# Kernel optimization log

Hardware: AMD Instinct MI355X
Metric: run time of the kernel (lower is better)

Reference implementation:

```python
import jax, jax.numpy as jnp
import numpy as np


def setup_inputs() -> dict:
    key = jax.random.key(0)
    ks = jax.random.split(key, 5)
    B, T, D, U = 32, 2048, 512, 512
    scale = 1.0 / np.sqrt(D)
    return {
        "full": jax.random.normal(ks[0], (B, T, D), jnp.float32),
        "last": jax.random.normal(ks[1], (B, D), jnp.float32),
        "W1": jax.random.normal(ks[2], (D, U), jnp.float32) * scale,
        "b1": jnp.zeros((U,), jnp.float32),
        "W2": jax.random.normal(ks[3], (D, U), jnp.float32) * scale,
        "b2": jnp.zeros((U,), jnp.float32),
        "V": jax.random.normal(ks[4], (U, 1), jnp.float32) * (1.0 / np.sqrt(U)),
        "bV": jnp.zeros((1,), jnp.float32),
    }


def reference(full, last, W1, b1, W2, b2, V, bV):
    # full: [B,T,D], last: [B,D]
    h1 = jnp.einsum("btd,du->btu", full, W1) + b1          # [B,T,U]
    h2 = last @ W2 + b2                                      # [B,U]
    score = jnp.tanh(h1 + h2[:, None, :]) @ V + bV           # [B,T,1]
    attn = jax.nn.softmax(score, axis=1)                     # [B,T,1]
    context = jnp.sum(attn * full, axis=1)                   # [B,D]
    return context
```

## Files before the change

### kernel.cpp

```cpp
#include <hip/hip_runtime.h>
#include <math.h>


#define BB 32
#define TT 2048
#define DD 512
#define UU 512

typedef short bf16x8 __attribute__((ext_vector_type(8)));
typedef float f32x4  __attribute__((ext_vector_type(4)));

static __device__ __forceinline__ short f2bf(float f) {
    unsigned x = __float_as_uint(f);
    return (short)((x + 0x7fffu + ((x >> 16) & 1u)) >> 16);
}

static __device__ __forceinline__ float fast_tanh(float x) {
    float e = __expf(2.f * x);
    return 1.f - 2.f * __builtin_amdgcn_rcpf(e + 1.f);
}

__global__ __launch_bounds__(256) void prep_kernel(const float* __restrict__ W1,
                                                   short* __restrict__ W1T,
                                                   const float* __restrict__ last,
                                                   const float* __restrict__ W2,
                                                   const float* __restrict__ b1,
                                                   const float* __restrict__ b2,
                                                   float* __restrict__ h2) {
    __shared__ float tile[32][33];
    __shared__ float ls[DD];
    const int bid = blockIdx.x;
    const int tid = threadIdx.x;
    if (bid < 256) {
        const int tr = (bid >> 4) << 5;
        const int tc = (bid & 15) << 5;
#pragma unroll
        for (int p = 0; p < 4; ++p) {
            const int r = p * 8 + (tid >> 5), c = tid & 31;
            tile[r][c] = W1[(size_t)(tr + r) * UU + tc + c];
        }
        __syncthreads();
#pragma unroll
        for (int p = 0; p < 4; ++p) {
            const int r = p * 8 + (tid >> 5), c = tid & 31;
            W1T[(size_t)(tc + r) * DD + tr + c] = f2bf(tile[c][r]);
        }
    } else {
        const int b = bid - 256;
        for (int i = tid; i < DD; i += 256) ls[i] = last[b * DD + i];
        __syncthreads();
        float a0 = 0.f, a1 = 0.f;
#pragma unroll 8
        for (int d = 0; d < DD; ++d) {
            const float l = ls[d];
            a0 += l * W2[d * UU + tid];
            a1 += l * W2[d * UU + tid + 256];
        }
        h2[b * UU + tid]       = a0 + b1[tid] + b2[tid];
        h2[b * UU + tid + 256] = a1 + b1[tid + 256] + b2[tid + 256];
    }
}

__global__ __launch_bounds__(256, 2) void score_kernel(const float* __restrict__ full,
                                                       const short* __restrict__ W1T,
                                                       const float* __restrict__ h2,
                                                       const float* __restrict__ V,
                                                       float* __restrict__ scores) {
    __shared__ __align__(16) short a_lds[1024 * 8];
    __shared__ float score_red[4][64];

    const int bid = blockIdx.x;
    const int b  = bid >> 5;
    const int t0 = (bid & 31) << 6;
    const int tid = threadIdx.x;
    const int w    = tid >> 6;
    const int lane = tid & 63;
    const int quad = lane >> 4;
    const int col  = lane & 15;

    f32x4 acc[4][8];
#pragma unroll
    for (int i = 0; i < 4; ++i)
#pragma unroll
        for (int j = 0; j < 8; ++j) acc[i][j] = (f32x4){0.f, 0.f, 0.f, 0.f};

    const size_t fullbase = (size_t)(b * TT + t0) * DD;
    const short* bbase = W1T + (size_t)(w * 128 + col) * DD + quad * 8;

    for (int ko = 0; ko < 4; ++ko) {
        if (ko > 0) __syncthreads();
#pragma unroll
        for (int i = 0; i < 4; ++i) {
            const int id  = tid + 256 * i;
            const int row = id >> 4;
            const int cc  = (id & 15) ^ (row & 15);
            const float* src = &full[fullbase + (size_t)row * DD + ko * 128 + cc * 8];
            const float4 v0 = *(const float4*)src;
            const float4 v1 = *(const float4*)(src + 4);
            bf16x8 pk = {f2bf(v0.x), f2bf(v0.y), f2bf(v0.z), f2bf(v0.w),
                         f2bf(v1.x), f2bf(v1.y), f2bf(v1.z), f2bf(v1.w)};
            *(bf16x8*)&a_lds[id * 8] = pk;
        }
        __syncthreads();

        for (int ki = 0; ki < 4; ++ki) {
            bf16x8 af[4];
#pragma unroll
            for (int mt = 0; mt < 4; ++mt) {
                const int row = mt * 16 + col;
                const int sl  = row * 16 + ((ki * 4 + quad) ^ col);
                af[mt] = *(const bf16x8*)&a_lds[sl * 8];
            }
            const int kg = ko * 128 + ki * 32;
#pragma unroll
            for (int nt = 0; nt < 8; ++nt) {
                const bf16x8 bf = *(const bf16x8*)&bbase[(size_t)nt * 16 * DD + kg];
#pragma unroll
                for (int mt = 0; mt < 4; ++mt)
                    acc[mt][nt] = __builtin_amdgcn_mfma_f32_16x16x32_bf16(af[mt], bf, acc[mt][nt], 0, 0, 0);
            }
        }
    }

    float srow[16];
#pragma unroll
    for (int i = 0; i < 16; ++i) srow[i] = 0.f;
#pragma unroll
    for (int nt = 0; nt < 8; ++nt) {
        const int u = w * 128 + nt * 16 + col;
        const float hv = h2[b * UU + u];
        const float vv = V[u];
#pragma unroll
        for (int mt = 0; mt < 4; ++mt)
#pragma unroll
            for (int r = 0; r < 4; ++r)
                srow[mt * 4 + r] += fast_tanh(acc[mt][nt][r] + hv) * vv;
    }
#pragma unroll
    for (int off = 1; off < 16; off <<= 1) {
#pragma unroll
        for (int i = 0; i < 16; ++i) srow[i] += __shfl_xor(srow[i], off, 64);
    }
    if (col == 0) {
#pragma unroll
        for (int mt = 0; mt < 4; ++mt)
#pragma unroll
            for (int r = 0; r < 4; ++r)
                score_red[w][mt * 16 + quad * 4 + r] = srow[mt * 4 + r];
    }
    __syncthreads();
    if (tid < 64)
        scores[b * TT + t0 + tid] = score_red[0][tid] + score_red[1][tid] +
                                    score_red[2][tid] + score_red[3][tid];
}

__global__ __launch_bounds__(256) void softmax_kernel(float* __restrict__ scores,
                                                      float* __restrict__ out) {
    const int b = blockIdx.x;
    const int tid = threadIdx.x;
    __shared__ float red[256];

    out[b * DD + tid] = 0.f;
    out[b * DD + 256 + tid] = 0.f;

    float local[8];
    float m = -1e30f;
#pragma unroll
    for (int i = 0; i < 8; ++i) {
        local[i] = scores[b * TT + i * 256 + tid];
        m = fmaxf(m, local[i]);
    }
    red[tid] = m;
    __syncthreads();
    for (int s = 128; s > 0; s >>= 1) {
        if (tid < s) red[tid] = fmaxf(red[tid], red[tid + s]);
        __syncthreads();
    }
    const float mx = red[0];
    __syncthreads();

    float sum = 0.f;
#pragma unroll
    for (int i = 0; i < 8; ++i) {
        local[i] = __expf(local[i] - mx);
        sum += local[i];
    }
    red[tid] = sum;
    __syncthreads();
    for (int s = 128; s > 0; s >>= 1) {
        if (tid < s) red[tid] += red[tid + s];
        __syncthreads();
    }
    const float inv = 1.f / red[0];
#pragma unroll
    for (int i = 0; i < 8; ++i) scores[b * TT + i * 256 + tid] = local[i] * inv;
}

__global__ __launch_bounds__(256) void context_kernel(const float* __restrict__ full,
                                                      const float* __restrict__ p,
                                                      float* __restrict__ out) {
    const int bid = blockIdx.x;
    const int b  = bid >> 3;
    const int d0 = ((bid >> 1) & 3) * 128;
    const int t0 = (bid & 1) * 1024;
    const int tid = threadIdx.x;
    const int c  = tid & 31;
    const int tr = tid >> 5;

    __shared__ float ps[1024];
    __shared__ float4 red[256];
    for (int i = tid; i < 1024; i += 256) ps[i] = p[b * TT + t0 + i];
    __syncthreads();

    float ax = 0.f, ay = 0.f, az = 0.f, aw = 0.f;
    const float* base = full + ((size_t)(b * TT + t0)) * DD + d0;
#pragma unroll 4
    for (int it = 0; it < 128; ++it) {
        const int t = it * 8 + tr;
        const float4 v = *(const float4*)&base[(size_t)t * DD + c * 4];
        const float wg = ps[t];
        ax += wg * v.x; ay += wg * v.y; az += wg * v.z; aw += wg * v.w;
    }
    red[tid] = make_float4(ax, ay, az, aw);
    __syncthreads();
    if (tid < 32) {
        float4 s = red[tid];
#pragma unroll
        for (int g = 1; g < 8; ++g) {
            const float4 o = red[g * 32 + tid];
            s.x += o.x; s.y += o.y; s.z += o.z; s.w += o.w;
        }
        atomicAdd(&out[b * DD + d0 + tid * 4 + 0], s.x);
        atomicAdd(&out[b * DD + d0 + tid * 4 + 1], s.y);
        atomicAdd(&out[b * DD + d0 + tid * 4 + 2], s.z);
        atomicAdd(&out[b * DD + d0 + tid * 4 + 3], s.w);
    }
}

extern "C" void kernel_launch(void* const* d_in, const int* in_sizes, int n_in,
                              void* d_out, int out_size, void* d_ws, size_t ws_size,
                              hipStream_t stream) {
    const float* full = (const float*)d_in[0];
    const float* last = (const float*)d_in[1];
    const float* W1   = (const float*)d_in[2];
    const float* b1   = (const float*)d_in[3];
    const float* W2   = (const float*)d_in[4];
    const float* b2   = (const float*)d_in[5];
    const float* V    = (const float*)d_in[6];

    float* out    = (float*)d_out;
    float* scores = (float*)d_ws;
    float* h2     = (float*)d_ws + (size_t)BB * TT;
    short* W1T    = (short*)(h2 + (size_t)BB * UU);

    prep_kernel<<<256 + BB, 256, 0, stream>>>(W1, W1T, last, W2, b1, b2, h2);
    score_kernel<<<BB * (TT / 64), 256, 0, stream>>>(full, W1T, h2, V, scores);
    softmax_kernel<<<BB, 256, 0, stream>>>(scores, out);
    context_kernel<<<256, 256, 0, stream>>>(full, scores, out);
}
```

Measured before the change: 314.9 us.

## Stage A and W1 tiles via direct global-to-LDS loads; fuse softmax into context

The score GEMM now loads fp32 activation tiles and bf16 W1T tiles straight into LDS with global_load_lds using XOR-swizzled layouts. The k-step shrinks to 32, and the bf16 conversion of activations moves to after the LDS read. Before, B fragments were read directly from global memory and activations were converted in registers before the LDS store. The separate softmax kernel is removed: each context block recomputes the row max and exp-sum itself, and the output is zeroed with a memset. This saves a launch and a pass over the scores, at the cost of redundant softmax work and 16 barriers per tile in place of 4.

```diff
diff --git a/kernel.cpp b/kernel.cpp
--- a/kernel.cpp
+++ b/kernel.cpp
@@ -66,7 +66,8 @@
                                                        const float* __restrict__ h2,
                                                        const float* __restrict__ V,
                                                        float* __restrict__ scores) {
-    __shared__ __align__(16) short a_lds[1024 * 8];
+    __shared__ __align__(16) float a32[64 * 32];
+    __shared__ __align__(16) short blds[512 * 32];
     __shared__ float score_red[4][64];
 
     const int bid = blockIdx.x;
@@ -85,40 +86,50 @@
         for (int j = 0; j < 8; ++j) acc[i][j] = (f32x4){0.f, 0.f, 0.f, 0.f};
 
     const size_t fullbase = (size_t)(b * TT + t0) * DD;
-    const short* bbase = W1T + (size_t)(w * 128 + col) * DD + quad * 8;
-
-    for (int ko = 0; ko < 4; ++ko) {
-        if (ko > 0) __syncthreads();
-#pragma unroll
-        for (int i = 0; i < 4; ++i) {
-            const int id  = tid + 256 * i;
-            const int row = id >> 4;
-            const int cc  = (id & 15) ^ (row & 15);
-            const float* src = &full[fullbase + (size_t)row * DD + ko * 128 + cc * 8];
-            const float4 v0 = *(const float4*)src;
-            const float4 v1 = *(const float4*)(src + 4);
-            bf16x8 pk = {f2bf(v0.x), f2bf(v0.y), f2bf(v0.z), f2bf(v0.w),
-                         f2bf(v1.x), f2bf(v1.y), f2bf(v1.z), f2bf(v1.w)};
-            *(bf16x8*)&a_lds[id * 8] = pk;
-        }
-        __syncthreads();
-
-        for (int ki = 0; ki < 4; ++ki) {
-            bf16x8 af[4];
-#pragma unroll
-            for (int mt = 0; mt < 4; ++mt) {
-                const int row = mt * 16 + col;
-                const int sl  = row * 16 + ((ki * 4 + quad) ^ col);
-                af[mt] = *(const bf16x8*)&a_lds[sl * 8];
-            }
-            const int kg = ko * 128 + ki * 32;
-#pragma unroll
-            for (int nt = 0; nt < 8; ++nt) {
-                const bf16x8 bf = *(const bf16x8*)&bbase[(size_t)nt * 16 * DD + kg];
-#pragma unroll
-                for (int mt = 0; mt < 4; ++mt)
-                    acc[mt][nt] = __builtin_amdgcn_mfma_f32_16x16x32_bf16(af[mt], bf, acc[mt][nt], 0, 0, 0);
-            }
+
+    for (int ko = 0; ko < 16; ++ko) {
+        if (ko) __syncthreads();
+#pragma unroll
+        for (int i = 0; i < 2; ++i) {
+            const int id = w * 128 + i * 64 + lane;
+            const int r  = id >> 3;
+            const int cc = (id & 7) ^ (r & 7);
+            const float* g = &full[fullbase + (size_t)r * DD + ko * 32 + cc * 4];
+            __builtin_amdgcn_global_load_lds(
+                (const __attribute__((address_space(1))) void*)g,
+                (__attribute__((address_space(3))) void*)&a32[(w * 128 + i * 64) * 4],
+                16, 0, 0);
+        }
+#pragma unroll
+        for (int i = 0; i < 8; ++i) {
+            const int id = w * 512 + i * 64 + lane;
+            const int u  = id >> 2;
+            const int kc = (id & 3) ^ (u & 3) ^ ((u >> 2) & 3);
+            const short* g = &W1T[(size_t)u * DD + ko * 32 + kc * 8];
+            __builtin_amdgcn_global_load_lds(
+                (const __attribute__((address_space(1))) void*)g,
+                (__attribute__((address_space(3))) void*)&blds[(w * 512 + i * 64) * 8],
+                16, 0, 0);
+        }
+        __syncthreads();
+
+        bf16x8 af[4];
+#pragma unroll
+        for (int mt = 0; mt < 4; ++mt) {
+            const int r = mt * 16 + col;
+            const f32x4 lo = *(const f32x4*)&a32[(r * 8 + ((quad * 2 + 0) ^ (r & 7))) * 4];
+            const f32x4 hi = *(const f32x4*)&a32[(r * 8 + ((quad * 2 + 1) ^ (r & 7))) * 4];
+            af[mt] = (bf16x8){f2bf(lo.x), f2bf(lo.y), f2bf(lo.z), f2bf(lo.w),
+                              f2bf(hi.x), f2bf(hi.y), f2bf(hi.z), f2bf(hi.w)};
+        }
+#pragma unroll
+        for (int nt = 0; nt < 8; ++nt) {
+            const int u  = w * 128 + nt * 16 + col;
+            const int sl = u * 4 + (quad ^ (u & 3) ^ ((u >> 2) & 3));
+            const bf16x8 bf = *(const bf16x8*)&blds[sl * 8];
+#pragma unroll
+            for (int mt = 0; mt < 4; ++mt)
+                acc[mt][nt] = __builtin_amdgcn_mfma_f32_16x16x32_bf16(af[mt], bf, acc[mt][nt], 0, 0, 0);
         }
     }
 
@@ -154,50 +165,8 @@
                                     score_red[2][tid] + score_red[3][tid];
 }
 
-__global__ __launch_bounds__(256) void softmax_kernel(float* __restrict__ scores,
-                                                      float* __restrict__ out) {
-    const int b = blockIdx.x;
-    const int tid = threadIdx.x;
-    __shared__ float red[256];
-
-    out[b * DD + tid] = 0.f;
-    out[b * DD + 256 + tid] = 0.f;
-
-    float local[8];
-    float m = -1e30f;
-#pragma unroll
-    for (int i = 0; i < 8; ++i) {
-        local[i] = scores[b * TT + i * 256 + tid];
-        m = fmaxf(m, local[i]);
-    }
-    red[tid] = m;
-    __syncthreads();
-    for (int s = 128; s > 0; s >>= 1) {
-        if (tid < s) red[tid] = fmaxf(red[tid], red[tid + s]);
-        __syncthreads();
-    }
-    const float mx = red[0];
-    __syncthreads();
-
-    float sum = 0.f;
-#pragma unroll
-    for (int i = 0; i < 8; ++i) {
-        local[i] = __expf(local[i] - mx);
-        sum += local[i];
-    }
-    red[tid] = sum;
-    __syncthreads();
-    for (int s = 128; s > 0; s >>= 1) {
-        if (tid < s) red[tid] += red[tid + s];
-        __syncthreads();
-    }
-    const float inv = 1.f / red[0];
-#pragma unroll
-    for (int i = 0; i < 8; ++i) scores[b * TT + i * 256 + tid] = local[i] * inv;
-}
-
 __global__ __launch_bounds__(256) void context_kernel(const float* __restrict__ full,
-                                                      const float* __restrict__ p,
+                                                      const float* __restrict__ scores,
                                                       float* __restrict__ out) {
     const int bid = blockIdx.x;
     const int b  = bid >> 3;
@@ -207,10 +176,43 @@
     const int c  = tid & 31;
     const int tr = tid >> 5;
 
+    __shared__ float red[256];
     __shared__ float ps[1024];
-    __shared__ float4 red[256];
-    for (int i = tid; i < 1024; i += 256) ps[i] = p[b * TT + t0 + i];
-    __syncthreads();
+    __shared__ float4 red4[256];
+
+    float local[8];
+    float m = -1e30f;
+#pragma unroll
+    for (int j = 0; j < 8; ++j) {
+        local[j] = scores[b * TT + j * 256 + tid];
+        m = fmaxf(m, local[j]);
+    }
+    red[tid] = m;
+    __syncthreads();
+    for (int s = 128; s > 0; s >>= 1) {
+        if (tid < s) red[tid] = fmaxf(red[tid], red[tid + s]);
+        __syncthreads();
+    }
+    const float mx = red[0];
+    __syncthreads();
+
+    float sum = 0.f;
+    float e[8];
+#pragma unroll
+    for (int j = 0; j < 8; ++j) {
+        e[j] = __expf(local[j] - mx);
+        sum += e[j];
+    }
+    const int jbase = t0 >> 8;
+#pragma unroll
+    for (int i = 0; i < 4; ++i) ps[i * 256 + tid] = e[jbase + i];
+    red[tid] = sum;
+    __syncthreads();
+    for (int s = 128; s > 0; s >>= 1) {
+        if (tid < s) red[tid] += red[tid + s];
+        __syncthreads();
+    }
+    const float inv = 1.f / red[0];
 
     float ax = 0.f, ay = 0.f, az = 0.f, aw = 0.f;
     const float* base = full + ((size_t)(b * TT + t0)) * DD + d0;
@@ -221,19 +223,19 @@
         const float wg = ps[t];
         ax += wg * v.x; ay += wg * v.y; az += wg * v.z; aw += wg * v.w;
     }
-    red[tid] = make_float4(ax, ay, az, aw);
+    red4[tid] = make_float4(ax, ay, az, aw);
     __syncthreads();
     if (tid < 32) {
-        float4 s = red[tid];
+        float4 s = red4[tid];
 #pragma unroll
         for (int g = 1; g < 8; ++g) {
-            const float4 o = red[g * 32 + tid];
+            const float4 o = red4[g * 32 + tid];
             s.x += o.x; s.y += o.y; s.z += o.z; s.w += o.w;
         }
-        atomicAdd(&out[b * DD + d0 + tid * 4 + 0], s.x);
-        atomicAdd(&out[b * DD + d0 + tid * 4 + 1], s.y);
-        atomicAdd(&out[b * DD + d0 + tid * 4 + 2], s.z);
-        atomicAdd(&out[b * DD + d0 + tid * 4 + 3], s.w);
+        atomicAdd(&out[b * DD + d0 + tid * 4 + 0], s.x * inv);
+        atomicAdd(&out[b * DD + d0 + tid * 4 + 1], s.y * inv);
+        atomicAdd(&out[b * DD + d0 + tid * 4 + 2], s.z * inv);
+        atomicAdd(&out[b * DD + d0 + tid * 4 + 3], s.w * inv);
     }
 }
 
@@ -253,8 +255,8 @@
     float* h2     = (float*)d_ws + (size_t)BB * TT;
     short* W1T    = (short*)(h2 + (size_t)BB * UU);
 
+    hipMemsetAsync(d_out, 0, (size_t)out_size * sizeof(float), stream);
     prep_kernel<<<256 + BB, 256, 0, stream>>>(W1, W1T, last, W2, b1, b2, h2);
     score_kernel<<<BB * (TT / 64), 256, 0, stream>>>(full, W1T, h2, V, scores);
-    softmax_kernel<<<BB, 256, 0, stream>>>(scores, out);
     context_kernel<<<256, 256, 0, stream>>>(full, scores, out);
 }
```

After: 300.1 us. -4.7%, faster.
